# Performance work log

Hardware: AMD Instinct MI355X
Metric: run time of the kernel (lower is better)

The kernel has to match this reference:

```python
import jax, jax.numpy as jnp
import numpy as np

HEADS, HD = 8, 64

def swish(x):
    return x * jax.nn.sigmoid(x)

def layer_norm(x, eps=1e-5):
    mu = jnp.mean(x, axis=-1, keepdims=True)
    var = jnp.var(x, axis=-1, keepdims=True)
    return (x - mu) / jnp.sqrt(var + eps)

def setup_inputs() -> dict:
    key = jax.random.key(0)
    k1, k2, k3 = jax.random.split(key, 3)
    B, L, D = 2, 2048, 512
    x = jax.random.normal(k1, (B, L, D), jnp.float32)
    cnn_w = jax.random.normal(k2, (HEADS * HD * 3, D, 3), jnp.float32) * 0.02
    cnn_b = jnp.zeros((HEADS * HD * 3,), jnp.float32)
    fc_w = jax.random.normal(k3, (D, HEADS * HD), jnp.float32) * 0.02
    fc_b = jnp.zeros((D,), jnp.float32)
    return {"x": x, "cnn_w": cnn_w, "cnn_b": cnn_b, "fc_w": fc_w, "fc_b": fc_b}

def reference(x, cnn_w, cnn_b, fc_w, fc_b):
    B, L, D = x.shape
    # Conv1d(dims -> heads*hd*3, kernel=3, stride=1, pad=1) on channel-first layout
    xt = jnp.transpose(x, (0, 2, 1))  # [B, D, L]
    y = jax.lax.conv_general_dilated(
        xt, cnn_w, window_strides=(1,), padding=[(1, 1)],
        dimension_numbers=("NCH", "OIH", "NCH"),
    ) + cnn_b[None, :, None]  # [B, 3*H*HD, L]
    qkv = swish(y).reshape(B, HEADS, HD * 3, L)
    q, k, v = jnp.split(qkv, 3, axis=-2)  # each [B, H, HD, L]
    # NOTE: original scales by sqrt(length), not sqrt(hd)
    scores = jnp.einsum("bhdw,bhdm->bhwm", q, k) / jnp.sqrt(jnp.float32(L))
    att = jax.nn.softmax(scores, axis=-1)  # [B, H, L, L]
    new_v = jnp.einsum("bhwm,bhdm->bwhd", att, v).reshape(B, L, HEADS * HD)
    m = swish(new_v @ fc_w.T + fc_b)  # [B, L, D]
    return layer_norm(x * 2 + m)
```

## Files before the change

### kernel.cpp

```cpp
#include <hip/hip_runtime.h>
#include <hip/hip_bf16.h>

#define BB 2
#define LL 2048
#define DD 512
#define HH 8
#define HDM 64
#define SCALE 0.022097086912079608f
#define QSCALE 0.03187935766f

typedef __hip_bfloat16 bf16;
typedef unsigned short u16;
typedef __attribute__((ext_vector_type(8))) short short8v;
typedef __attribute__((ext_vector_type(4))) float float4v;

#define XN  2097152
#define WN  2359296
#define BN  1536
#define FWN 262144
#define FBN 512

__device__ __forceinline__ float b2f(u16 u) {
    return __uint_as_float(((unsigned int)u) << 16);
}
__device__ __forceinline__ u16 f2u(float f) {
    bf16 h = __float2bfloat16(f);
    u16 r;
    __builtin_memcpy(&r, &h, 2);
    return r;
}
__device__ __forceinline__ uint4 pack8(const float* f) {
    uint4 p;
    p.x = (unsigned)f2u(f[0]) | ((unsigned)f2u(f[1]) << 16);
    p.y = (unsigned)f2u(f[2]) | ((unsigned)f2u(f[3]) << 16);
    p.z = (unsigned)f2u(f[4]) | ((unsigned)f2u(f[5]) << 16);
    p.w = (unsigned)f2u(f[6]) | ((unsigned)f2u(f[7]) << 16);
    return p;
}

__device__ __forceinline__ void gld_lds16(const u16* g, u16* l) {
    __builtin_amdgcn_global_load_lds(
        (const __attribute__((address_space(1))) unsigned int*)g,
        (__attribute__((address_space(3))) unsigned int*)l, 16, 0, 0);
}

__device__ __forceinline__ int detect_flag(const u16* __restrict__ xraw) {
    int bad = 0;
    int lane = threadIdx.x & 63;
    for (int i = lane; i < 256; i += 64) {
        float v = b2f(xraw[i]);
        if (!(fabsf(v) < 100.f)) bad = 1;
    }
    return (__ballot(bad) != 0ull) ? 1 : 0;
}

__device__ __forceinline__ void conv8(const void* src, u16* dst, size_t i, int flag) {
    if (flag) {
        const float* s = (const float*)src;
        float f[8];
        float4 a = *(const float4*)(s + i);
        float4 b = *(const float4*)(s + i + 4);
        f[0] = a.x; f[1] = a.y; f[2] = a.z; f[3] = a.w;
        f[4] = b.x; f[5] = b.y; f[6] = b.z; f[7] = b.w;
        *(uint4*)(dst + i) = pack8(f);
    } else {
        *(uint4*)(dst + i) = *(const uint4*)((const u16*)src + i);
    }
}

__global__ __launch_bounds__(256) void prep_kernel(
    const void* __restrict__ xsrc, const void* __restrict__ wsrc,
    const void* __restrict__ bsrc, const void* __restrict__ fwsrc,
    const void* __restrict__ fbsrc,
    u16* __restrict__ xp, u16* __restrict__ wt,
    u16* __restrict__ bc, u16* __restrict__ fwc, u16* __restrict__ fbc)
{
    const int flag = detect_flag((const u16*)xsrc);
    const int bid = blockIdx.x;

    if (bid < 1024) {
        int idx = bid * 256 + threadIdx.x;
        if (idx < 256) {
            int b2  = idx >> 7;
            int r2  = (idx >> 6) & 1;
            int c82 = (idx & 63) * 8;
            size_t off = ((size_t)(b2 * 2050 + (r2 ? 2049 : 0))) * 512 + c82;
            uint4 z = {0u, 0u, 0u, 0u};
            *(uint4*)(xp + off) = z;
        }
        int b   = idx / (LL * 64);
        int rem = idx - b * (LL * 64);
        int l   = rem >> 6;
        int c8  = (rem & 63) * 8;
        size_t si = ((size_t)(b * LL + l)) * 512 + c8;
        size_t di = ((size_t)(b * 2050 + l + 1)) * 512 + c8;
        if (flag) {
            const float* s = (const float*)xsrc;
            float f[8];
            float4 a = *(const float4*)(s + si);
            float4 bq = *(const float4*)(s + si + 4);
            f[0] = a.x; f[1] = a.y; f[2] = a.z; f[3] = a.w;
            f[4] = bq.x; f[5] = bq.y; f[6] = bq.z; f[7] = bq.w;
            *(uint4*)(xp + di) = pack8(f);
        } else {
            *(uint4*)(xp + di) = *(const uint4*)((const u16*)xsrc + si);
        }
    } else if (bid < 2176) {
        int idx = (bid - 1024) * 256 + threadIdx.x;
        int i8  = idx & 63;
        int rem = idx >> 6;
        int k   = rem % 3;
        int o   = rem / 3;
        float f[8];
        if (flag) {
            const float* s = (const float*)wsrc;
#pragma unroll
            for (int j = 0; j < 8; ++j) f[j] = s[(size_t)o * 1536 + (i8 * 8 + j) * 3 + k];
        } else {
            const u16* s = (const u16*)wsrc;
#pragma unroll
            for (int j = 0; j < 8; ++j) f[j] = b2f(s[(size_t)o * 1536 + (i8 * 8 + j) * 3 + k]);
        }
        *(uint4*)(wt + (size_t)o * 1536 + k * 512 + i8 * 8) = pack8(f);
    } else {
        int o = (bid - 2176) * 256 + threadIdx.x;
        if (o < BN / 8) {
            conv8(bsrc, bc, (size_t)o * 8, flag);
        } else if (o < BN / 8 + FWN / 8) {
            conv8(fwsrc, fwc, (size_t)(o - BN / 8) * 8, flag);
        } else if (o < BN / 8 + FWN / 8 + FBN / 8) {
            conv8(fbsrc, fbc, (size_t)(o - BN / 8 - FWN / 8) * 8, flag);
        }
    }
}

__global__ __launch_bounds__(256) void conv_mfma_kernel(
    const u16* __restrict__ xp,
    const u16* __restrict__ wt,
    const u16* __restrict__ bias,
    u16* __restrict__ qkbuf,
    u16* __restrict__ vbuf)
{
    __shared__ u16 smem[32768];
    u16* Asb = smem;
    u16* Bsb = smem + 2 * 128 * 64;
#define OTS 140
    u16* OT  = smem;

    const int blk = blockIdx.x;
    const int rt = blk / 12;
    const int ct = blk - rt * 12;
    const int b  = rt >> 4;
    const int l0 = (rt & 15) * 128;
    const int tid  = threadIdx.x;
    const int wave = tid >> 6;
    const int lane = tid & 63;
    const int quad = lane >> 4;
    const int l16  = lane & 15;
    const int e7   = l16 & 7;
    const int wx = wave & 1;
    const int wy = wave >> 1;

    float4v acc[4][4];
#pragma unroll
    for (int mt = 0; mt < 4; ++mt)
#pragma unroll
        for (int nt = 0; nt < 4; ++nt) acc[mt][nt] = (float4v){0.f, 0.f, 0.f, 0.f};

    const int rowW = wave * 32;
    const int lrow = lane >> 3;
    const int g8   = (((lane & 7) ^ lrow)) * 8;
    auto stage = [&](int kc, int buf) {
        const int slab = kc >> 3;
        const int i0   = (kc & 7) * 64;
        const u16* ga = xp + ((size_t)(b * 2050 + l0 + rowW + slab + lrow)) * 512 + i0 + g8;
        const u16* gb = wt + ((size_t)(ct * 128 + rowW + lrow)) * 1536 + kc * 64 + g8;
        u16* la = Asb + (size_t)(buf * 128 + rowW) * 64;
        u16* lb = Bsb + (size_t)(buf * 128 + rowW) * 64;
#pragma unroll
        for (int j = 0; j < 4; ++j) {
            gld_lds16(ga + (size_t)(j * 8) * 512,  la + (j * 8) * 64);
            gld_lds16(gb + (size_t)(j * 8) * 1536, lb + (j * 8) * 64);
        }
    };

    stage(0, 0);

    for (int kc = 0; kc < 24; ++kc) {
        const int cur = kc & 1;
        __syncthreads();

        if (kc < 23) stage(kc + 1, 1 - cur);

#pragma unroll
        for (int half = 0; half < 2; ++half) {
            const int p = ((half * 4 + quad) ^ e7) * 8;
            short8v aF[4], bF[4];
#pragma unroll
            for (int mt = 0; mt < 4; ++mt)
                aF[mt] = *(const short8v*)&Asb[(size_t)(cur * 128 + wy * 64 + mt * 16 + l16) * 64 + p];
#pragma unroll
            for (int nt = 0; nt < 4; ++nt)
                bF[nt] = *(const short8v*)&Bsb[(size_t)(cur * 128 + wx * 64 + nt * 16 + l16) * 64 + p];
#pragma unroll
            for (int mt = 0; mt < 4; ++mt)
#pragma unroll
                for (int nt = 0; nt < 4; ++nt)
                    acc[mt][nt] = __builtin_amdgcn_mfma_f32_16x16x32_bf16(
                        aF[mt], bF[nt], acc[mt][nt], 0, 0, 0);
        }
    }

    __syncthreads();
    {
        const int tloc = (ct * 2 + wx) % 3;
#pragma unroll
        for (int nt = 0; nt < 4; ++nt) {
            int oc = wx * 64 + nt * 16 + l16;
            float bb = b2f(bias[ct * 128 + oc]);
#pragma unroll
            for (int mt = 0; mt < 4; ++mt)
#pragma unroll
                for (int r = 0; r < 4; ++r) {
                    int lr = wy * 64 + mt * 16 + quad * 4 + r;
                    float y = acc[mt][nt][r] + bb;
                    y = y / (1.f + __expf(-y));
                    if (tloc == 0) y *= QSCALE;
                    OT[lr * OTS + oc] = f2u(y);
                }
        }
    }
    __syncthreads();

#pragma unroll
    for (int g = 0; g < 2; ++g) {
        int a  = ct * 2 + g;
        int t  = a % 3;
        int bh = b * HH + a / 3;
        if (t != 2) {
            u16* base = qkbuf + ((size_t)((bh * 2 + t) * LL + l0)) * HDM;
#pragma unroll
            for (int it = 0; it < 4; ++it) {
                int idx = it * 256 + tid;
                int l   = idx >> 3;
                int d8  = (idx & 7) * 8;
                uint4 val = *(const uint4*)&OT[l * OTS + g * 64 + d8];
                *(uint4*)(base + (size_t)l * HDM + d8) = val;
            }
        } else {
            u16* base = vbuf + ((size_t)(bh * HDM)) * LL + l0;
#pragma unroll
            for (int it = 0; it < 4; ++it) {
                int idx = it * 256 + tid;
                int dd  = idx >> 4;
                int p   = idx & 15;
                int l8  = p * 8;
                u16 tmp[8];
#pragma unroll
                for (int j = 0; j < 8; ++j) tmp[j] = OT[(l8 + j) * OTS + g * 64 + dd];
                int a32 = p >> 2;
                int pb_ = p & 3;
                int q2  = (2 * pb_) & 3;
                int h2  = pb_ >> 1;
                int n0  = 32 * a32 + 8 * q2 + 4 * h2;
                uint2 v0, v1;
                v0.x = (unsigned)tmp[0] | ((unsigned)tmp[1] << 16);
                v0.y = (unsigned)tmp[2] | ((unsigned)tmp[3] << 16);
                v1.x = (unsigned)tmp[4] | ((unsigned)tmp[5] << 16);
                v1.y = (unsigned)tmp[6] | ((unsigned)tmp[7] << 16);
                *(uint2*)(base + (size_t)dd * LL + n0)     = v0;
                *(uint2*)(base + (size_t)dd * LL + n0 + 8) = v1;
            }
        }
    }
#undef OTS
}

__global__ __launch_bounds__(256) void attn_mfma_kernel(
    const u16* __restrict__ qk,
    const u16* __restrict__ v,
    u16* __restrict__ newv)
{
    __shared__ u16 kts[2][128][64];
    __shared__ u16 vts[2][64][128];

    const int blkid = blockIdx.x;
    const int bh = blkid >> 5;
    const int wc = blkid & 31;
    const int b  = bh >> 3;
    const int h  = bh & 7;
    const int tid  = threadIdx.x;
    const int wave = tid >> 6;
    const int lane = tid & 63;
    const int quad = lane >> 4;
    const int l16  = lane & 15;
    const int e7   = l16 & 7;

    const u16* qbase = qk + ((size_t)(bh * 2 + 0)) * LL * HDM;
    const u16* kbase = qk + ((size_t)(bh * 2 + 1)) * LL * HDM;
    const u16* vbase = v + (size_t)bh * HDM * LL;

    const int w0 = wc * 64 + wave * 16;

    short8v qfrag[2];
    qfrag[0] = *(const short8v*)(qbase + (size_t)(w0 + l16) * HDM + quad * 8);
    qfrag[1] = *(const short8v*)(qbase + (size_t)(w0 + l16) * HDM + 32 + quad * 8);

    short8v vones;
    {
        short o1 = (l16 == 0) ? (short)0x3F80 : (short)0;
#pragma unroll
        for (int j = 0; j < 8; ++j) vones[j] = o1;
    }

    float4v oacc[4];
#pragma unroll
    for (int dt = 0; dt < 4; ++dt) oacc[dt] = (float4v){0.f, 0.f, 0.f, 0.f};
    float4v lacc = (float4v){0.f, 0.f, 0.f, 0.f};

    const int rbK   = wave * 32;
    const int lrowK = lane >> 3;
    const int gK    = ((lane & 7) ^ lrowK) * 8;
    const int rbV   = wave * 16;
    const int lrowV = lane >> 4;
    auto stage = [&](int ic, int buf) {
        const int m0 = ic * 128;
#pragma unroll
        for (int j = 0; j < 4; ++j) {
            gld_lds16(kbase + (size_t)(m0 + rbK + j * 8 + lrowK) * HDM + gK,
                      &kts[buf][rbK + j * 8][0]);
            const int vrow = j * 4 + lrowV;
            gld_lds16(vbase + (size_t)(rbV + vrow) * LL + m0 + (((lane & 15) ^ vrow) * 8),
                      &vts[buf][rbV + j * 4][0]);
        }
    };

    stage(0, 0);

    for (int ic = 0; ic < 16; ++ic) {
        const int cur = ic & 1;
        __syncthreads();

        if (ic < 15) stage(ic + 1, 1 - cur);

        float4v s[8];
#pragma unroll
        for (int mt = 0; mt < 8; ++mt) {
            s[mt] = (float4v){0.f, 0.f, 0.f, 0.f};
            short8v b0 = *(const short8v*)&kts[cur][mt * 16 + l16][((quad) ^ e7) * 8];
            s[mt] = __builtin_amdgcn_mfma_f32_16x16x32_bf16(b0, qfrag[0], s[mt], 0, 0, 0);
            short8v b1 = *(const short8v*)&kts[cur][mt * 16 + l16][((quad + 4) ^ e7) * 8];
            s[mt] = __builtin_amdgcn_mfma_f32_16x16x32_bf16(b1, qfrag[1], s[mt], 0, 0, 0);
        }

        unsigned pk[8][2];
#pragma unroll
        for (int mt = 0; mt < 8; ++mt) {
            float p0 = __builtin_amdgcn_exp2f(s[mt][0]);
            float p1 = __builtin_amdgcn_exp2f(s[mt][1]);
            float p2 = __builtin_amdgcn_exp2f(s[mt][2]);
            float p3 = __builtin_amdgcn_exp2f(s[mt][3]);
            pk[mt][0] = (unsigned)f2u(p0) | ((unsigned)f2u(p1) << 16);
            pk[mt][1] = (unsigned)f2u(p2) | ((unsigned)f2u(p3) << 16);
        }

#pragma unroll
        for (int mu = 0; mu < 4; ++mu) {
            union { short8v v8; unsigned u[4]; } U;
            U.u[0] = pk[2 * mu][0];
            U.u[1] = pk[2 * mu][1];
            U.u[2] = pk[2 * mu + 1][0];
            U.u[3] = pk[2 * mu + 1][1];
            const short8v pb = U.v8;

            lacc = __builtin_amdgcn_mfma_f32_16x16x32_bf16(vones, pb, lacc, 0, 0, 0);

#pragma unroll
            for (int dt = 0; dt < 4; ++dt) {
                short8v va = *(const short8v*)&vts[cur][dt * 16 + l16][((4 * mu + quad) ^ l16) * 8];
                oacc[dt] = __builtin_amdgcn_mfma_f32_16x16x32_bf16(va, pb, oacc[dt], 0, 0, 0);
            }
        }
    }

    float lsum = __shfl(lacc[0], l16);
    float inv = 1.f / lsum;
    u16* ob = newv + (size_t)b * LL * 512 + h * 64;
#pragma unroll
    for (int dt = 0; dt < 4; ++dt) {
        unsigned lo = (unsigned)f2u(oacc[dt][0] * inv) | ((unsigned)f2u(oacc[dt][1] * inv) << 16);
        unsigned hi = (unsigned)f2u(oacc[dt][2] * inv) | ((unsigned)f2u(oacc[dt][3] * inv) << 16);
        uint2 val; val.x = lo; val.y = hi;
        *(uint2*)(ob + (size_t)(w0 + l16) * 512 + dt * 16 + quad * 4) = val;
    }
}

__global__ __launch_bounds__(256) void fc_ln_mfma_kernel(
    const u16* __restrict__ newv,
    const u16* __restrict__ fcw,
    const u16* __restrict__ fcb,
    const u16* __restrict__ xp,
    const u16* __restrict__ xraw,
    void* __restrict__ out)
{
    const int flag = detect_flag(xraw);
    const int l0 = blockIdx.x * 16;
    const int tid  = threadIdx.x;
    const int wave = tid >> 6;
    const int lane = tid & 63;
    const int quad = lane >> 4;
    const int l16  = lane & 15;
    const int col0 = wave * 128;

    const int bb_ = l0 >> 11;
    const size_t xbase = ((size_t)(bb_ * 2050 + (l0 & 2047) + 1)) * 512;

    __shared__ float psum[4][16], psq[4][16];

    short8v aF[16];
    const u16* arow = newv + (size_t)(l0 + l16) * 512 + quad * 8;
#pragma unroll
    for (int kc = 0; kc < 16; ++kc)
        aF[kc] = *(const short8v*)(arow + kc * 32);

    float4v acc[8];
#pragma unroll
    for (int nt = 0; nt < 8; ++nt) acc[nt] = (float4v){0.f, 0.f, 0.f, 0.f};

#pragma unroll
    for (int nt = 0; nt < 8; ++nt) {
        const u16* brow = fcw + (size_t)(col0 + nt * 16 + l16) * 512 + quad * 8;
#pragma unroll
        for (int kc = 0; kc < 16; ++kc) {
            short8v bF = *(const short8v*)(brow + kc * 32);
            acc[nt] = __builtin_amdgcn_mfma_f32_16x16x32_bf16(aF[kc], bF, acc[nt], 0, 0, 0);
        }
    }

    float z[8][4];
    float rs[4] = {0.f, 0.f, 0.f, 0.f}, rq[4] = {0.f, 0.f, 0.f, 0.f};
#pragma unroll
    for (int nt = 0; nt < 8; ++nt) {
        int col = col0 + nt * 16 + l16;
        float bb = b2f(fcb[col]);
#pragma unroll
        for (int r = 0; r < 4; ++r) {
            int row = quad * 4 + r;
            float y = acc[nt][r] + bb;
            float sw = y / (1.f + __expf(-y));
            float xv = b2f(xp[xbase + (size_t)row * 512 + col]);
            float zz = xv * 2.f + sw;
            z[nt][r] = zz;
            rs[r] += zz;
            rq[r] += zz * zz;
        }
    }
#pragma unroll
    for (int msk = 1; msk <= 8; msk <<= 1)
#pragma unroll
        for (int r = 0; r < 4; ++r) {
            rs[r] += __shfl_xor(rs[r], msk);
            rq[r] += __shfl_xor(rq[r], msk);
        }
    if (l16 == 0) {
#pragma unroll
        for (int r = 0; r < 4; ++r) {
            psum[wave][quad * 4 + r] = rs[r];
            psq[wave][quad * 4 + r]  = rq[r];
        }
    }
    __syncthreads();

    float mu[4], inv[4];
#pragma unroll
    for (int r = 0; r < 4; ++r) {
        int row = quad * 4 + r;
        float s = psum[0][row] + psum[1][row] + psum[2][row] + psum[3][row];
        float q = psq[0][row] + psq[1][row] + psq[2][row] + psq[3][row];
        float m = s * (1.f / 512.f);
        float var = q * (1.f / 512.f) - m * m;
        mu[r] = m;
        inv[r] = rsqrtf(var + 1e-5f);
    }

#pragma unroll
    for (int nt = 0; nt < 8; ++nt) {
        int col = col0 + nt * 16 + l16;
#pragma unroll
        for (int r = 0; r < 4; ++r) {
            int row = quad * 4 + r;
            float val = (z[nt][r] - mu[r]) * inv[r];
            if (flag) ((float*)out)[(size_t)(l0 + row) * 512 + col] = val;
            else      ((u16*)out)[(size_t)(l0 + row) * 512 + col] = f2u(val);
        }
    }
}

extern "C" void kernel_launch(void* const* d_in, const int* in_sizes, int n_in,
                              void* d_out, int out_size, void* d_ws, size_t ws_size,
                              hipStream_t stream) {
    (void)in_sizes; (void)n_in; (void)out_size; (void)ws_size;

    char* ws = (char*)d_ws;
    u16* xp   = (u16*)(ws + 256);
    u16* wtc  = (u16*)(ws + 4198656);
    u16* bc   = (u16*)(ws + 8917248);
    u16* fwc  = (u16*)(ws + 8920320);
    u16* fbc  = (u16*)(ws + 9444608);
    u16* qkb  = (u16*)(ws + 9445632);
    u16* vb   = (u16*)(ws + 17834240);
    u16* nvc  = (u16*)(ws + 22028544);

    prep_kernel<<<dim3(2305), dim3(256), 0, stream>>>(
        d_in[0], d_in[1], d_in[2], d_in[3], d_in[4],
        xp, wtc, bc, fwc, fbc);

    conv_mfma_kernel<<<dim3(32 * 12), dim3(256), 0, stream>>>(xp, wtc, bc, qkb, vb);
    attn_mfma_kernel<<<dim3(BB * HH * (LL / 64)), dim3(256), 0, stream>>>(qkb, vb, nvc);
    fc_ln_mfma_kernel<<<dim3(256), dim3(256), 0, stream>>>(
        nvc, fwc, fbc, xp, (const u16*)d_in[0], d_out);
}
```

Baseline: 162.4 us.

## Split attention keys across two wave groups with larger query tiles per block

The attention kernel now uses 512-thread blocks covering 128 queries each, with every wave handling two 16-row query subtiles so each K/V fragment read from shared memory feeds twice as many MFMAs. The eight waves form two key groups that process alternating 64-key chunks. Their partial outputs and softmax denominators are combined through shared memory at the end. Block IDs are remapped to interleave heads across the grid. The intent is to reduce LDS traffic per MFMA and improve latency hiding, at the cost of fewer blocks (256), more registers per thread and an extra reduction phase.

```diff
diff --git a/kernel.cpp b/kernel.cpp
--- a/kernel.cpp
+++ b/kernel.cpp
@@ -276,21 +276,24 @@
 #undef OTS
 }
 
-__global__ __launch_bounds__(256) void attn_mfma_kernel(
+__global__ __launch_bounds__(512) void attn_mfma_kernel(
     const u16* __restrict__ qk,
     const u16* __restrict__ v,
     u16* __restrict__ newv)
 {
-    __shared__ u16 kts[2][128][64];
-    __shared__ u16 vts[2][64][128];
-
-    const int blkid = blockIdx.x;
-    const int bh = blkid >> 5;
-    const int wc = blkid & 31;
+    __shared__ u16 smem[32768];
+    u16 (*kts)[2][64][64] = (u16 (*)[2][64][64])smem;
+    u16 (*vts)[2][64][64] = (u16 (*)[2][64][64])(smem + 16384);
+
+    const int lb = ((blockIdx.x & 7) << 5) + (blockIdx.x >> 3);
+    const int bh = lb >> 4;
+    const int qc = lb & 15;
     const int b  = bh >> 3;
     const int h  = bh & 7;
     const int tid  = threadIdx.x;
     const int wave = tid >> 6;
+    const int kg   = wave >> 2;
+    const int qg   = wave & 3;
     const int lane = tid & 63;
     const int quad = lane >> 4;
     const int l16  = lane & 15;
@@ -300,11 +303,15 @@
     const u16* kbase = qk + ((size_t)(bh * 2 + 1)) * LL * HDM;
     const u16* vbase = v + (size_t)bh * HDM * LL;
 
-    const int w0 = wc * 64 + wave * 16;
-
-    short8v qfrag[2];
-    qfrag[0] = *(const short8v*)(qbase + (size_t)(w0 + l16) * HDM + quad * 8);
-    qfrag[1] = *(const short8v*)(qbase + (size_t)(w0 + l16) * HDM + 32 + quad * 8);
+    const int q0 = qc * 128 + qg * 32;
+
+    short8v qfrag[2][2];
+#pragma unroll
+    for (int sg = 0; sg < 2; ++sg) {
+        const u16* qr = qbase + (size_t)(q0 + sg * 16 + l16) * HDM + quad * 8;
+        qfrag[sg][0] = *(const short8v*)(qr);
+        qfrag[sg][1] = *(const short8v*)(qr + 32);
+    }
 
     short8v vones;
     {
@@ -313,85 +320,123 @@
         for (int j = 0; j < 8; ++j) vones[j] = o1;
     }
 
-    float4v oacc[4];
-#pragma unroll
-    for (int dt = 0; dt < 4; ++dt) oacc[dt] = (float4v){0.f, 0.f, 0.f, 0.f};
-    float4v lacc = (float4v){0.f, 0.f, 0.f, 0.f};
-
-    const int rbK   = wave * 32;
-    const int lrowK = lane >> 3;
-    const int gK    = ((lane & 7) ^ lrowK) * 8;
-    const int rbV   = wave * 16;
-    const int lrowV = lane >> 4;
+    float4v oacc[2][4];
+    float4v lacc[2];
+#pragma unroll
+    for (int sg = 0; sg < 2; ++sg) {
+        lacc[sg] = (float4v){0.f, 0.f, 0.f, 0.f};
+#pragma unroll
+        for (int dt = 0; dt < 4; ++dt) oacc[sg][dt] = (float4v){0.f, 0.f, 0.f, 0.f};
+    }
+
+    const int rr  = qg * 8 + (lane >> 3);
+    const int sw8 = ((lane & 7) ^ (lane >> 3)) * 8;
     auto stage = [&](int ic, int buf) {
-        const int m0 = ic * 128;
-#pragma unroll
-        for (int j = 0; j < 4; ++j) {
-            gld_lds16(kbase + (size_t)(m0 + rbK + j * 8 + lrowK) * HDM + gK,
-                      &kts[buf][rbK + j * 8][0]);
-            const int vrow = j * 4 + lrowV;
-            gld_lds16(vbase + (size_t)(rbV + vrow) * LL + m0 + (((lane & 15) ^ vrow) * 8),
-                      &vts[buf][rbV + j * 4][0]);
+        const int m0 = ic * 64;
+#pragma unroll
+        for (int r = 0; r < 2; ++r) {
+            gld_lds16(kbase + (size_t)(m0 + r * 32 + rr) * HDM + sw8,
+                      &kts[kg][buf][r * 32 + qg * 8][0]);
+            gld_lds16(vbase + (size_t)(r * 32 + rr) * LL + m0 + sw8,
+                      &vts[kg][buf][r * 32 + qg * 8][0]);
         }
     };
 
-    stage(0, 0);
-
-    for (int ic = 0; ic < 16; ++ic) {
-        const int cur = ic & 1;
+    stage(kg, 0);
+
+    for (int i = 0; i < 16; ++i) {
+        const int cur = i & 1;
         __syncthreads();
 
-        if (ic < 15) stage(ic + 1, 1 - cur);
-
-        float4v s[8];
-#pragma unroll
-        for (int mt = 0; mt < 8; ++mt) {
-            s[mt] = (float4v){0.f, 0.f, 0.f, 0.f};
-            short8v b0 = *(const short8v*)&kts[cur][mt * 16 + l16][((quad) ^ e7) * 8];
-            s[mt] = __builtin_amdgcn_mfma_f32_16x16x32_bf16(b0, qfrag[0], s[mt], 0, 0, 0);
-            short8v b1 = *(const short8v*)&kts[cur][mt * 16 + l16][((quad + 4) ^ e7) * 8];
-            s[mt] = __builtin_amdgcn_mfma_f32_16x16x32_bf16(b1, qfrag[1], s[mt], 0, 0, 0);
-        }
-
-        unsigned pk[8][2];
-#pragma unroll
-        for (int mt = 0; mt < 8; ++mt) {
-            float p0 = __builtin_amdgcn_exp2f(s[mt][0]);
-            float p1 = __builtin_amdgcn_exp2f(s[mt][1]);
-            float p2 = __builtin_amdgcn_exp2f(s[mt][2]);
-            float p3 = __builtin_amdgcn_exp2f(s[mt][3]);
-            pk[mt][0] = (unsigned)f2u(p0) | ((unsigned)f2u(p1) << 16);
-            pk[mt][1] = (unsigned)f2u(p2) | ((unsigned)f2u(p3) << 16);
-        }
-
-#pragma unroll
-        for (int mu = 0; mu < 4; ++mu) {
-            union { short8v v8; unsigned u[4]; } U;
-            U.u[0] = pk[2 * mu][0];
-            U.u[1] = pk[2 * mu][1];
-            U.u[2] = pk[2 * mu + 1][0];
-            U.u[3] = pk[2 * mu + 1][1];
-            const short8v pb = U.v8;
-
-            lacc = __builtin_amdgcn_mfma_f32_16x16x32_bf16(vones, pb, lacc, 0, 0, 0);
-
+        if (i < 15) stage(2 * (i + 1) + kg, 1 - cur);
+
+        float4v s[2][4];
+#pragma unroll
+        for (int mt = 0; mt < 4; ++mt) {
+            short8v b0 = *(const short8v*)&kts[kg][cur][mt * 16 + l16][((quad) ^ e7) * 8];
+            short8v b1 = *(const short8v*)&kts[kg][cur][mt * 16 + l16][((quad + 4) ^ e7) * 8];
+#pragma unroll
+            for (int sg = 0; sg < 2; ++sg) {
+                float4v t = (float4v){0.f, 0.f, 0.f, 0.f};
+                t = __builtin_amdgcn_mfma_f32_16x16x32_bf16(b0, qfrag[sg][0], t, 0, 0, 0);
+                t = __builtin_amdgcn_mfma_f32_16x16x32_bf16(b1, qfrag[sg][1], t, 0, 0, 0);
+                s[sg][mt] = t;
+            }
+        }
+
+        unsigned pk[2][4][2];
+#pragma unroll
+        for (int sg = 0; sg < 2; ++sg)
+#pragma unroll
+            for (int mt = 0; mt < 4; ++mt) {
+                float p0 = __builtin_amdgcn_exp2f(s[sg][mt][0]);
+                float p1 = __builtin_amdgcn_exp2f(s[sg][mt][1]);
+                float p2 = __builtin_amdgcn_exp2f(s[sg][mt][2]);
+                float p3 = __builtin_amdgcn_exp2f(s[sg][mt][3]);
+                pk[sg][mt][0] = (unsigned)f2u(p0) | ((unsigned)f2u(p1) << 16);
+                pk[sg][mt][1] = (unsigned)f2u(p2) | ((unsigned)f2u(p3) << 16);
+            }
+
+#pragma unroll
+        for (int mu = 0; mu < 2; ++mu) {
+            short8v pb[2];
+#pragma unroll
+            for (int sg = 0; sg < 2; ++sg) {
+                union { short8v v8; unsigned u[4]; } U;
+                U.u[0] = pk[sg][2 * mu][0];
+                U.u[1] = pk[sg][2 * mu][1];
+                U.u[2] = pk[sg][2 * mu + 1][0];
+                U.u[3] = pk[sg][2 * mu + 1][1];
+                pb[sg] = U.v8;
+                lacc[sg] = __builtin_amdgcn_mfma_f32_16x16x32_bf16(vones, pb[sg], lacc[sg], 0, 0, 0);
+            }
 #pragma unroll
             for (int dt = 0; dt < 4; ++dt) {
-                short8v va = *(const short8v*)&vts[cur][dt * 16 + l16][((4 * mu + quad) ^ l16) * 8];
-                oacc[dt] = __builtin_amdgcn_mfma_f32_16x16x32_bf16(va, pb, oacc[dt], 0, 0, 0);
-            }
-        }
-    }
-
-    float lsum = __shfl(lacc[0], l16);
-    float inv = 1.f / lsum;
-    u16* ob = newv + (size_t)b * LL * 512 + h * 64;
-#pragma unroll
-    for (int dt = 0; dt < 4; ++dt) {
-        unsigned lo = (unsigned)f2u(oacc[dt][0] * inv) | ((unsigned)f2u(oacc[dt][1] * inv) << 16);
-        unsigned hi = (unsigned)f2u(oacc[dt][2] * inv) | ((unsigned)f2u(oacc[dt][3] * inv) << 16);
-        uint2 val; val.x = lo; val.y = hi;
-        *(uint2*)(ob + (size_t)(w0 + l16) * 512 + dt * 16 + quad * 4) = val;
+                short8v va = *(const short8v*)&vts[kg][cur][dt * 16 + l16][((mu * 4 + quad) ^ e7) * 8];
+#pragma unroll
+                for (int sg = 0; sg < 2; ++sg)
+                    oacc[sg][dt] = __builtin_amdgcn_mfma_f32_16x16x32_bf16(va, pb[sg], oacc[sg][dt], 0, 0, 0);
+            }
+        }
+    }
+
+    float dnm[2];
+#pragma unroll
+    for (int sg = 0; sg < 2; ++sg) dnm[sg] = __shfl(lacc[sg][0], l16);
+
+    __syncthreads();
+    float* xch = (float*)smem;
+    if (kg == 1) {
+#pragma unroll
+        for (int sg = 0; sg < 2; ++sg) {
+#pragma unroll
+            for (int dt = 0; dt < 4; ++dt)
+#pragma unroll
+                for (int r = 0; r < 4; ++r)
+                    xch[((qg * 34 + (sg * 16 + dt * 4 + r)) << 6) + lane] = oacc[sg][dt][r];
+            xch[((qg * 34 + 32 + sg) << 6) + lane] = dnm[sg];
+        }
+    }
+    __syncthreads();
+    if (kg == 0) {
+        u16* ob = newv + (size_t)b * LL * 512 + h * 64;
+#pragma unroll
+        for (int sg = 0; sg < 2; ++sg) {
+            float dt2 = dnm[sg] + xch[((qg * 34 + 32 + sg) << 6) + lane];
+            float inv = 1.f / dt2;
+            const size_t orow = (size_t)(q0 + sg * 16 + l16) * 512 + quad * 4;
+#pragma unroll
+            for (int dt = 0; dt < 4; ++dt) {
+                float o0 = oacc[sg][dt][0] + xch[((qg * 34 + (sg * 16 + dt * 4 + 0)) << 6) + lane];
+                float o1 = oacc[sg][dt][1] + xch[((qg * 34 + (sg * 16 + dt * 4 + 1)) << 6) + lane];
+                float o2 = oacc[sg][dt][2] + xch[((qg * 34 + (sg * 16 + dt * 4 + 2)) << 6) + lane];
+                float o3 = oacc[sg][dt][3] + xch[((qg * 34 + (sg * 16 + dt * 4 + 3)) << 6) + lane];
+                unsigned lo = (unsigned)f2u(o0 * inv) | ((unsigned)f2u(o1 * inv) << 16);
+                unsigned hi = (unsigned)f2u(o2 * inv) | ((unsigned)f2u(o3 * inv) << 16);
+                uint2 val; val.x = lo; val.y = hi;
+                *(uint2*)(ob + orow + dt * 16) = val;
+            }
+        }
     }
 }
 
@@ -516,7 +561,7 @@
         xp, wtc, bc, fwc, fbc);
 
     conv_mfma_kernel<<<dim3(32 * 12), dim3(256), 0, stream>>>(xp, wtc, bc, qkb, vb);
-    attn_mfma_kernel<<<dim3(BB * HH * (LL / 64)), dim3(256), 0, stream>>>(qkb, vb, nvc);
+    attn_mfma_kernel<<<dim3(256), dim3(512), 0, stream>>>(qkb, vb, nvc);
     fc_ln_mfma_kernel<<<dim3(256), dim3(256), 0, stream>>>(
         nvc, fwc, fbc, xp, (const u16*)d_in[0], d_out);
 }
```

After: 154.9 us. 4.6% less time.
